# Performance work log

Measured on AMD Instinct MI355X. Metric: run time of the kernel, lower is better.

## Reference

```python
import jax, jax.numpy as jnp
import numpy as np

EPS = 1e-5
RS = 2                 # trilinear sampling points per bin per dim (fixed sampling_ratio)
OUT_SIZE = (4, 7, 7)   # (T_out, H_out, W_out)


def hswish(x):
    return x * jnp.clip(x + 3.0, 0.0, 6.0) / 6.0


def bn3d(x, g, b, m, v):
    # eval-mode BatchNorm3d over channel dim 1 of [N,C,T,H,W]
    s = g * jax.lax.rsqrt(v + EPS)
    return x * s[None, :, None, None, None] + (b - m * s)[None, :, None, None, None]


def conv3d(x, w, stride=1, pad=0, groups=1):
    return jax.lax.conv_general_dilated(
        x, w, window_strides=(stride,) * 3, padding=[(pad, pad)] * 3,
        dimension_numbers=('NCDHW', 'OIDHW', 'NCDHW'), feature_group_count=groups)


def roi_align_3d(feat, start, end):
    # feat: [N,C,T,H,W]; start/end: [N,3] in (x, y, t) order (one ROI per sample)
    N, C, T, H, W = feat.shape
    Pt, Ph, Pw = OUT_SIZE

    def coords(s, e, P):
        size = jnp.maximum(e - s, 1.0)
        # flattened sample j = bin*RS + i -> position s + (j+0.5)/RS * bin_size
        offs = (jnp.arange(P * RS, dtype=feat.dtype) + 0.5) / RS
        return s[:, None] + offs[None, :] * (size / P)[:, None]  # [N, P*RS]

    cx = coords(start[:, 0], end[:, 0], Pw)
    cy = coords(start[:, 1], end[:, 1], Ph)
    ct = coords(start[:, 2], end[:, 2], Pt)

    def lin(v, c, L):
        # linear interpolation of v along its last axis at continuous coords c
        c = jnp.clip(c, 0.0, L - 1.0)
        lo = jnp.floor(c).astype(jnp.int32)
        hi = jnp.minimum(lo + 1, L - 1)
        w = c - lo.astype(c.dtype)
        return v[..., lo] * (1.0 - w) + v[..., hi] * w

    def one(f, tt, ty, tx):
        f = lin(f, tx, W)                   # [C,T,H,Sw]
        f = jnp.moveaxis(f, 2, -1)          # [C,T,Sw,H]
        f = lin(f, ty, H)                   # [C,T,Sw,Sh]
        f = jnp.moveaxis(f, 1, -1)          # [C,Sw,Sh,T]
        f = lin(f, tt, T)                   # [C,Sw,Sh,St]
        f = jnp.transpose(f, (0, 3, 2, 1))  # [C,St,Sh,Sw]
        f = f.reshape(f.shape[0], Pt, RS, Ph, RS, Pw, RS)
        return f.mean(axis=(2, 4, 6))       # average sample points per bin

    return jax.vmap(one)(feat, ct, cy, cx)  # [N,C,Pt,Ph,Pw]


def setup_inputs():
    key = jax.random.key(0)
    ks = jax.random.split(key, 9)
    N, Cin, T, H, W = 64, 256, 8, 16, 16
    Cr = 128

    def bn_params(k, c):
        k1, k2, k3, k4 = jax.random.split(k, 4)
        g = jax.random.uniform(k1, (c,), minval=0.5, maxval=1.5)
        b = 0.1 * jax.random.normal(k2, (c,))
        m = 0.1 * jax.random.normal(k3, (c,))
        v = jax.random.uniform(k4, (c,), minval=0.5, maxval=1.5)
        return g, b, m, v

    x = jax.random.normal(ks[0], (N, Cin, T, H, W), jnp.float32)
    w1 = jax.random.normal(ks[1], (Cr, Cin, 1, 1, 1)) / np.float32(np.sqrt(Cin))
    wdw = jax.random.normal(ks[2], (Cr, 1, 3, 3, 3)) / np.float32(np.sqrt(27))
    w2 = jax.random.normal(ks[3], (Cr, Cr, 1, 1, 1)) / np.float32(np.sqrt(Cr))
    w3 = jax.random.normal(ks[4], (6, Cr, 1, 1, 1)) / np.float32(np.sqrt(Cr))
    g1, b1, m1, v1 = bn_params(ks[5], Cr)
    g2, b2, m2, v2 = bn_params(ks[6], Cr)
    g3, b3, m3, v3 = bn_params(ks[7], Cr)
    g4, b4, m4, v4 = bn_params(ks[8], 6)
    return dict(x=x, w1=w1, g1=g1, b1=b1, m1=m1, v1=v1,
                wdw=wdw, g2=g2, b2=b2, m2=m2, v2=v2,
                w2=w2, g3=g3, b3=b3, m3=m3, v3=v3,
                w3=w3, g4=g4, b4=b4, m4=m4, v4=v4)


def reference(x, w1, g1, b1, m1, v1, wdw, g2, b2, m2, v2,
              w2, g3, b3, m3, v3, w3, g4, b4, m4, v4):
    N, C, T, H, W = x.shape
    h = hswish(bn3d(conv3d(x, w1), g1, b1, m1, v1))
    h = hswish(bn3d(conv3d(h, wdw, stride=2, pad=1, groups=wdw.shape[0]), g2, b2, m2, v2))
    h = hswish(bn3d(conv3d(h, w2), g3, b3, m3, v3))
    # AvgPool3d with kernel == reduced feature size -> global spatial-temporal mean
    h = jnp.mean(h, axis=(2, 3, 4), keepdims=True)
    logits = bn3d(conv3d(h, w3), g4, b4, m4, v4).reshape(N, 6)
    lim = jax.nn.sigmoid(logits)   # eval path (gumbel only in training)
    scales = jnp.array([W, H, T], dtype=x.dtype)      # (x, y, t) order
    start = 0.5 * lim[:, :3] * scales
    end = (1.0 - 0.5 * lim[:, 3:]) * scales
    return roi_align_3d(x, start, end)
```

## Files before the change

### kernel.cpp

```cpp
#include <hip/hip_runtime.h>
#include <math.h>

#define N_BATCH 64
#define CIN 256
#define CR 128
#define T_IN 8
#define H_IN 16
#define W_IN 16
#define S1 2048
#define T2 4
#define H2 8
#define W2 8
#define S2 256
#define PT 4
#define PH 7
#define PW 7
#define EPSB 1e-5f

typedef __attribute__((ext_vector_type(8))) short bf16x8;
typedef __attribute__((ext_vector_type(4))) float f32x4;
typedef __attribute__((ext_vector_type(4))) unsigned int u32x4;
typedef __attribute__((ext_vector_type(8))) unsigned short ushort8;

__device__ __forceinline__ float hswish(float y) {
    float c = fminf(fmaxf(y + 3.0f, 0.0f), 6.0f);
    return y * c * (1.0f / 6.0f);
}

__device__ __forceinline__ unsigned int fbits(float x) {
    return __float_as_uint(x);
}

__device__ __forceinline__ unsigned int pkbf16(float lo, float hi) {
    return ((fbits(lo) + 0x8000u) >> 16) | ((fbits(hi) + 0x8000u) & 0xFFFF0000u);
}

__global__ __launch_bounds__(256) void wsplit_kernel(
    const float* __restrict__ w1, unsigned short* __restrict__ whi,
    unsigned short* __restrict__ wlo, float* __restrict__ pp)
{
    int i = blockIdx.x * 256 + threadIdx.x;
    int co = i >> 8;
    int k  = i & 255;
    float x = w1[i];
    unsigned int bx = fbits(x);
    unsigned int h = (bx + 0x8000u) & 0xFFFF0000u;
    float r = x - __uint_as_float(h);
    int flat = ((((co >> 4) * 8 + (k >> 5)) * 4 + ((k >> 3) & 3)) * 16 + (co & 15)) * 8 + (k & 7);
    whi[flat] = (unsigned short)(h >> 16);
    wlo[flat] = (unsigned short)((fbits(r) + 0x8000u) >> 16);
    pp[i] = 0.0f;
}

#define BFIDX(g, h, e, ln) (((((g) * 2 + (h)) * 2 + (e)) * 16 + (ln)) * 4)

__global__ __launch_bounds__(256, 5) void conv1_mfma_kernel(
    const float* __restrict__ x,
    const unsigned short* __restrict__ whi, const unsigned short* __restrict__ wlo,
    const float* __restrict__ g, const float* __restrict__ b,
    const float* __restrict__ m, const float* __restrict__ v,
    unsigned short* __restrict__ h1b)
{
    __shared__ unsigned int Bf[2][1024];

    int blk = blockIdx.x;
    int n  = blk >> 5;
    int s0 = (blk & 31) << 6;
    int tid = threadIdx.x;
    int wave = tid >> 6;
    int lane = tid & 63;
    int gl   = lane >> 4;
    int ln16 = lane & 15;
    int hw   = wave & 1;
    int wcoG = (wave >> 1) * 4;

    int sg = tid >> 6;
    int sc = tid & 63;
    int sh = sc >> 5;
    int se = sc & 1;
    int sl = (sc & 31) >> 1;
    int wslot = BFIDX(sg, sh, se, sl);
    const float* xg = x + (size_t)n * CIN * S1 + s0 + sc;

    f32x4 acc[4][2];
    #pragma unroll
    for (int i = 0; i < 4; i++) {
        acc[i][0] = (f32x4){0.f, 0.f, 0.f, 0.f};
        acc[i][1] = (f32x4){0.f, 0.f, 0.f, 0.f};
    }

    float val[3][8];
    #pragma unroll
    for (int j = 0; j < 8; j++)
        val[0][j] = xg[(size_t)(sg * 8 + j) * S1];
    #pragma unroll
    for (int j = 0; j < 8; j++)
        val[1][j] = xg[(size_t)(32 + sg * 8 + j) * S1];
    {
        u32x4 wv;
        #pragma unroll
        for (int p = 0; p < 4; p++)
            wv[p] = pkbf16(val[0][2 * p], val[0][2 * p + 1]);
        *reinterpret_cast<u32x4*>(&Bf[0][wslot]) = wv;
    }
    __syncthreads();

    #pragma unroll
    for (int ks = 0; ks < 8; ks++) {
        bf16x8 Ah[4], Al[4];
        #pragma unroll
        for (int fc = 0; fc < 4; fc++) {
            int off = ((((wcoG + fc) * 8 + ks) * 4 + gl) * 16 + ln16) * 8;
            Ah[fc] = *reinterpret_cast<const bf16x8*>(whi + off);
            Al[fc] = *reinterpret_cast<const bf16x8*>(wlo + off);
        }
        if (ks < 6) {
            #pragma unroll
            for (int j = 0; j < 8; j++)
                val[(ks + 2) % 3][j] = xg[(size_t)((ks + 2) * 32 + sg * 8 + j) * S1];
        }
        if (ks < 7) {
            u32x4 wv;
            #pragma unroll
            for (int p = 0; p < 4; p++)
                wv[p] = pkbf16(val[(ks + 1) % 3][2 * p], val[(ks + 1) % 3][2 * p + 1]);
            *reinterpret_cast<u32x4*>(&Bf[(ks + 1) & 1][wslot]) = wv;
        }
        union { u32x4 u; bf16x8 bv; } B0, B1;
        B0.u = *reinterpret_cast<const u32x4*>(&Bf[ks & 1][BFIDX(gl, hw, 0, ln16)]);
        B1.u = *reinterpret_cast<const u32x4*>(&Bf[ks & 1][BFIDX(gl, hw, 1, ln16)]);
        #pragma unroll
        for (int fc = 0; fc < 4; fc++) {
            acc[fc][0] = __builtin_amdgcn_mfma_f32_16x16x32_bf16(Ah[fc], B0.bv, acc[fc][0], 0, 0, 0);
            acc[fc][1] = __builtin_amdgcn_mfma_f32_16x16x32_bf16(Ah[fc], B1.bv, acc[fc][1], 0, 0, 0);
        }
        #pragma unroll
        for (int fc = 0; fc < 4; fc++) {
            acc[fc][0] = __builtin_amdgcn_mfma_f32_16x16x32_bf16(Al[fc], B0.bv, acc[fc][0], 0, 0, 0);
            acc[fc][1] = __builtin_amdgcn_mfma_f32_16x16x32_bf16(Al[fc], B1.bv, acc[fc][1], 0, 0, 0);
        }
        if (ks < 7) __syncthreads();
    }

    #pragma unroll
    for (int fc = 0; fc < 4; fc++)
        #pragma unroll
        for (int reg = 0; reg < 4; reg++) {
            int co = (wcoG + fc) * 16 + gl * 4 + reg;
            float sc_ = g[co] * rsqrtf(v[co] + EPSB);
            float tt = fmaf(-m[co], sc_, b[co]);
            float y0 = hswish(fmaf(acc[fc][0][reg], sc_, tt));
            float y1 = hswish(fmaf(acc[fc][1][reg], sc_, tt));
            unsigned int pk = pkbf16(y0, y1);
            *reinterpret_cast<unsigned int*>(
                h1b + ((size_t)n * CR + co) * S1 + s0 + hw * 32 + ln16 * 2) = pk;
        }
}

__global__ __launch_bounds__(256) void dwconv_kernel(
    const unsigned short* __restrict__ h1b, const float* __restrict__ wdw,
    const float* __restrict__ g, const float* __restrict__ b,
    const float* __restrict__ m, const float* __restrict__ v,
    float* __restrict__ h2)
{
    __shared__ float s[T_IN][H_IN][W_IN];
    __shared__ float wl[27];
    int blk = blockIdx.x;
    int n = blk >> 7;
    int c = blk & 127;
    int tid = threadIdx.x;
    const unsigned short* in = h1b + ((size_t)n * CR + c) * S1;

    {
        int e = tid * 8;
        ushort8 u = *reinterpret_cast<const ushort8*>(in + e);
        float* sp = &s[0][0][0] + e;
        #pragma unroll
        for (int i = 0; i < 8; i++)
            sp[i] = __uint_as_float((unsigned int)(unsigned short)u[i] << 16);
    }
    if (tid < 27) wl[tid] = wdw[c * 27 + tid];
    __syncthreads();

    int wo = tid & 7;
    int ho = (tid >> 3) & 7;
    int to = tid >> 6;
    float acc = 0.0f;
    #pragma unroll
    for (int dt = 0; dt < 3; dt++) {
        int ti = 2 * to - 1 + dt;
        if (ti < 0 || ti >= T_IN) continue;
        #pragma unroll
        for (int dh = 0; dh < 3; dh++) {
            int hi = 2 * ho - 1 + dh;
            if (hi < 0 || hi >= H_IN) continue;
            #pragma unroll
            for (int dw = 0; dw < 3; dw++) {
                int wi = 2 * wo - 1 + dw;
                if (wi < 0 || wi >= W_IN) continue;
                acc = fmaf(wl[(dt * 3 + dh) * 3 + dw], s[ti][hi][wi], acc);
            }
        }
    }
    float sc = g[c] * rsqrtf(v[c] + EPSB);
    float y  = fmaf(acc, sc, fmaf(-m[c], sc, b[c]));
    h2[((size_t)n * CR + c) * S2 + tid] = hswish(y);
}

#define KC 16
__global__ __launch_bounds__(256) void conv2_kernel(
    const float* __restrict__ h2, const float* __restrict__ w2,
    const float* __restrict__ g, const float* __restrict__ b,
    const float* __restrict__ m, const float* __restrict__ v,
    float* __restrict__ pp)
{
    __shared__ float Xs[KC][64];
    __shared__ float Ws[KC][CR + 4];

    int blk = blockIdx.x;
    int n  = blk >> 2;
    int sq = blk & 3;
    int s0 = sq << 6;
    int tid = threadIdx.x;
    int tco = tid >> 3;
    int ts  = tid & 7;
    const float* xn = h2 + (size_t)n * CR * S2;

    float acc[4][8];
    #pragma unroll
    for (int i = 0; i < 4; i++)
        #pragma unroll
        for (int j = 0; j < 8; j++) acc[i][j] = 0.0f;

    for (int k0 = 0; k0 < CR; k0 += KC) {
        {
            int e  = tid * 4;
            int kk = e >> 6;
            int ss = e & 63;
            float4 xv = *reinterpret_cast<const float4*>(xn + (size_t)(k0 + kk) * S2 + s0 + ss);
            *reinterpret_cast<float4*>(&Xs[kk][ss]) = xv;
        }
        #pragma unroll
        for (int r = 0; r < 8; r++) {
            int e  = tid + r * 256;
            int co = e >> 4;
            int kk = e & 15;
            Ws[kk][co] = w2[co * CR + k0 + kk];
        }
        __syncthreads();
        #pragma unroll
        for (int kk = 0; kk < KC; kk++) {
            float a[4], bb[8];
            #pragma unroll
            for (int r = 0; r < 4; r++) a[r] = Ws[kk][tco * 4 + r];
            #pragma unroll
            for (int q = 0; q < 8; q++) bb[q] = Xs[kk][ts * 8 + q];
            #pragma unroll
            for (int r = 0; r < 4; r++)
                #pragma unroll
                for (int q = 0; q < 8; q++)
                    acc[r][q] = fmaf(a[r], bb[q], acc[r][q]);
        }
        __syncthreads();
    }

    #pragma unroll
    for (int r = 0; r < 4; r++) {
        int co = tco * 4 + r;
        float sc = g[co] * rsqrtf(v[co] + EPSB);
        float tt = fmaf(-m[co], sc, b[co]);
        float psum = 0.0f;
        #pragma unroll
        for (int q = 0; q < 8; q++)
            psum += hswish(fmaf(acc[r][q], sc, tt));
        #pragma unroll
        for (int off = 4; off > 0; off >>= 1)
            psum += __shfl_down(psum, off, 8);
        if (ts == 0)
            pp[((size_t)n * CR + co) * 4 + sq] = psum;
    }
}

__global__ __launch_bounds__(128) void head_kernel(
    const float* __restrict__ pp, const float* __restrict__ w3,
    const float* __restrict__ g, const float* __restrict__ b,
    const float* __restrict__ m, const float* __restrict__ v,
    float* __restrict__ boxes)
{
    __shared__ float red[2];
    int n = blockIdx.x;
    int c = threadIdx.x;
    int wave = c >> 6, lane = c & 63;
    const float* p = pp + ((size_t)n * CR + c) * 4;
    float pc = (p[0] + p[1] + p[2] + p[3]) * (1.0f / 256.0f);

    for (int j = 0; j < 6; j++) {
        float t = w3[j * CR + c] * pc;
        #pragma unroll
        for (int off = 32; off > 0; off >>= 1)
            t += __shfl_down(t, off, 64);
        if (lane == 0) red[wave] = t;
        __syncthreads();
        if (c == 0) {
            float acc = red[0] + red[1];
            float sc = g[j] * rsqrtf(v[j] + EPSB);
            float logit = fmaf(acc, sc, fmaf(-m[j], sc, b[j]));
            float lim = 1.0f / (1.0f + expf(-logit));
            float scale = ((j % 3) == 2) ? 8.0f : 16.0f;
            float val = (j < 3) ? 0.5f * lim * scale : (1.0f - 0.5f * lim) * scale;
            boxes[n * 6 + j] = val;
        }
        __syncthreads();
    }
}

__global__ __launch_bounds__(256) void roi_kernel(
    const float* __restrict__ x, const float* __restrict__ boxes,
    float* __restrict__ out)
{
    __shared__ float s[T_IN][H_IN][W_IN];
    __shared__ float box[6];
    int blk = blockIdx.x;
    int n = blk >> 8;
    int c = blk & 255;
    int tid = threadIdx.x;
    const float* in = x + ((size_t)n * CIN + c) * S1;
    #pragma unroll
    for (int r = 0; r < 2; r++) {
        int e = (tid + r * 256) * 4;
        *reinterpret_cast<float4*>(&s[0][0][0] + e) =
            *reinterpret_cast<const float4*>(in + e);
    }
    if (tid < 6) box[tid] = boxes[n * 6 + tid];
    __syncthreads();

    if (tid < PT * PH * PW) {
        int pw = tid % 7;
        int ph = (tid / 7) % 7;
        int pt = tid / 49;
        float sx = box[0], sy = box[1], st = box[2];
        float bszx = fmaxf(box[3] - sx, 1.0f) * (1.0f / PW);
        float bszy = fmaxf(box[4] - sy, 1.0f) * (1.0f / PH);
        float bszt = fmaxf(box[5] - st, 1.0f) * (1.0f / PT);

        float acc = 0.0f;
        #pragma unroll
        for (int it = 0; it < 2; it++) {
            float tc = st + ((float)(pt * 2 + it) + 0.5f) * 0.5f * bszt;
            tc = fminf(fmaxf(tc, 0.0f), (float)(T_IN - 1));
            int tlo = (int)floorf(tc);
            int thi = min(tlo + 1, T_IN - 1);
            float tw = tc - (float)tlo;
            #pragma unroll
            for (int iy = 0; iy < 2; iy++) {
                float yc = sy + ((float)(ph * 2 + iy) + 0.5f) * 0.5f * bszy;
                yc = fminf(fmaxf(yc, 0.0f), (float)(H_IN - 1));
                int ylo = (int)floorf(yc);
                int yhi = min(ylo + 1, H_IN - 1);
                float yw = yc - (float)ylo;
                #pragma unroll
                for (int ix = 0; ix < 2; ix++) {
                    float xc = sx + ((float)(pw * 2 + ix) + 0.5f) * 0.5f * bszx;
                    xc = fminf(fmaxf(xc, 0.0f), (float)(W_IN - 1));
                    int xlo = (int)floorf(xc);
                    int xhi = min(xlo + 1, W_IN - 1);
                    float xw = xc - (float)xlo;

                    float v00 = s[tlo][ylo][xlo] * (1.0f - xw) + s[tlo][ylo][xhi] * xw;
                    float v01 = s[tlo][yhi][xlo] * (1.0f - xw) + s[tlo][yhi][xhi] * xw;
                    float v10 = s[thi][ylo][xlo] * (1.0f - xw) + s[thi][ylo][xhi] * xw;
                    float v11 = s[thi][yhi][xlo] * (1.0f - xw) + s[thi][yhi][xhi] * xw;
                    float v0 = v00 * (1.0f - yw) + v01 * yw;
                    float v1 = v10 * (1.0f - yw) + v11 * yw;
                    acc += v0 * (1.0f - tw) + v1 * tw;
                }
            }
        }
        out[(((size_t)(n * CIN + c) * PT + pt) * PH + ph) * PW + pw] = acc * 0.125f;
    }
}

extern "C" void kernel_launch(void* const* d_in, const int* in_sizes, int n_in,
                              void* d_out, int out_size, void* d_ws, size_t ws_size,
                              hipStream_t stream) {
    const float* x   = (const float*)d_in[0];
    const float* w1  = (const float*)d_in[1];
    const float* g1  = (const float*)d_in[2];
    const float* b1  = (const float*)d_in[3];
    const float* m1  = (const float*)d_in[4];
    const float* v1  = (const float*)d_in[5];
    const float* wdw = (const float*)d_in[6];
    const float* g2  = (const float*)d_in[7];
    const float* b2  = (const float*)d_in[8];
    const float* m2  = (const float*)d_in[9];
    const float* v2  = (const float*)d_in[10];
    const float* w2  = (const float*)d_in[11];
    const float* g3  = (const float*)d_in[12];
    const float* b3  = (const float*)d_in[13];
    const float* m3  = (const float*)d_in[14];
    const float* v3  = (const float*)d_in[15];
    const float* w3  = (const float*)d_in[16];
    const float* g4  = (const float*)d_in[17];
    const float* b4  = (const float*)d_in[18];
    const float* m4  = (const float*)d_in[19];
    const float* v4  = (const float*)d_in[20];

    float* ws = (float*)d_ws;
    float* h1     = ws;
    float* h2     = h1 + (size_t)N_BATCH * CR * S1;
    float* h3     = h2 + (size_t)N_BATCH * CR * S2;
    float* pp     = h3 + (size_t)N_BATCH * CR * S2;
    float* boxes  = pp + (size_t)N_BATCH * CR * 4;
    unsigned short* h1b = (unsigned short*)h1;
    unsigned short* whi = (unsigned short*)h3;
    unsigned short* wlo = whi + CR * CIN;

    wsplit_kernel<<<dim3(128), dim3(256), 0, stream>>>(w1, whi, wlo, pp);
    conv1_mfma_kernel<<<dim3(2048), dim3(256), 0, stream>>>(x, whi, wlo, g1, b1, m1, v1, h1b);
    dwconv_kernel<<<dim3(N_BATCH * CR), dim3(256), 0, stream>>>(h1b, wdw, g2, b2, m2, v2, h2);
    conv2_kernel<<<dim3(256), dim3(256), 0, stream>>>(h2, w2, g3, b3, m3, v3, pp);
    head_kernel<<<dim3(N_BATCH), dim3(128), 0, stream>>>(pp, w3, g4, b4, m4, v4, boxes);
    roi_kernel<<<dim3(N_BATCH * CIN), dim3(256), 0, stream>>>(x, boxes, (float*)d_out);
}
```

Measured before the change: 125.3 us.

## Pre-convert input to channel-packed bf16 layout and drop LDS staging in conv1

Adds a separate kernel that converts x from fp32 into bf16 packed in groups of 8 channels per spatial position. conv1 then loads its MFMA B operands straight from global memory, with no shared-memory double buffering and no barriers. The aim is to remove the strided fp32 loads, the in-loop packing and the synchronisation from conv1. In exchange it adds a kernel launch plus an extra full write and read of x in bf16 (about 67MB of fp32 read and 33MB written), lowers the occupancy hint from 5 to 4, and repacks the workspace layout.

New measurement: 152.7 us. 21.9% more time.

```diff
diff --git a/kernel.cpp b/kernel.cpp
--- a/kernel.cpp
+++ b/kernel.cpp
@@ -52,17 +52,37 @@
     pp[i] = 0.0f;
 }
 
-#define BFIDX(g, h, e, ln) (((((g) * 2 + (h)) * 2 + (e)) * 16 + (ln)) * 4)
-
-__global__ __launch_bounds__(256, 5) void conv1_mfma_kernel(
-    const float* __restrict__ x,
+__global__ __launch_bounds__(256) void xcvt_kernel(
+    const float* __restrict__ x, unsigned short* __restrict__ xb8)
+{
+    int blk = blockIdx.x;
+    int n   = blk >> 5;
+    int ci8 = blk & 31;
+    int t = threadIdx.x;
+    const float* xr = x + ((size_t)n * CIN + ci8 * 8) * S1;
+    unsigned short* ob = xb8 + (size_t)blk * S1 * 8;
+    #pragma unroll
+    for (int i = 0; i < 8; i++) {
+        int s = i * 256 + t;
+        float vj[8];
+        #pragma unroll
+        for (int j = 0; j < 8; j++)
+            vj[j] = xr[(size_t)j * S1 + s];
+        u32x4 pk;
+        #pragma unroll
+        for (int p = 0; p < 4; p++)
+            pk[p] = pkbf16(vj[2 * p], vj[2 * p + 1]);
+        *reinterpret_cast<u32x4*>(ob + (size_t)s * 8) = pk;
+    }
+}
+
+__global__ __launch_bounds__(256, 4) void conv1_mfma_kernel(
+    const unsigned short* __restrict__ xb8,
     const unsigned short* __restrict__ whi, const unsigned short* __restrict__ wlo,
     const float* __restrict__ g, const float* __restrict__ b,
     const float* __restrict__ m, const float* __restrict__ v,
     unsigned short* __restrict__ h1b)
 {
-    __shared__ unsigned int Bf[2][1024];
-
     int blk = blockIdx.x;
     int n  = blk >> 5;
     int s0 = (blk & 31) << 6;
@@ -74,13 +94,8 @@
     int hw   = wave & 1;
     int wcoG = (wave >> 1) * 4;
 
-    int sg = tid >> 6;
-    int sc = tid & 63;
-    int sh = sc >> 5;
-    int se = sc & 1;
-    int sl = (sc & 31) >> 1;
-    int wslot = BFIDX(sg, sh, se, sl);
-    const float* xg = x + (size_t)n * CIN * S1 + s0 + sc;
+    const unsigned short* xb = xb8 +
+        (((size_t)n * 32 + gl) * S1 + s0 + hw * 32 + 2 * ln16) * 8;
 
     f32x4 acc[4][2];
     #pragma unroll
@@ -89,24 +104,10 @@
         acc[i][1] = (f32x4){0.f, 0.f, 0.f, 0.f};
     }
 
-    float val[3][8];
-    #pragma unroll
-    for (int j = 0; j < 8; j++)
-        val[0][j] = xg[(size_t)(sg * 8 + j) * S1];
-    #pragma unroll
-    for (int j = 0; j < 8; j++)
-        val[1][j] = xg[(size_t)(32 + sg * 8 + j) * S1];
-    {
-        u32x4 wv;
-        #pragma unroll
-        for (int p = 0; p < 4; p++)
-            wv[p] = pkbf16(val[0][2 * p], val[0][2 * p + 1]);
-        *reinterpret_cast<u32x4*>(&Bf[0][wslot]) = wv;
-    }
-    __syncthreads();
-
     #pragma unroll
     for (int ks = 0; ks < 8; ks++) {
+        bf16x8 B0 = *reinterpret_cast<const bf16x8*>(xb + (size_t)(ks * 4) * S1 * 8);
+        bf16x8 B1 = *reinterpret_cast<const bf16x8*>(xb + (size_t)(ks * 4) * S1 * 8 + 8);
         bf16x8 Ah[4], Al[4];
         #pragma unroll
         for (int fc = 0; fc < 4; fc++) {
@@ -114,32 +115,16 @@
             Ah[fc] = *reinterpret_cast<const bf16x8*>(whi + off);
             Al[fc] = *reinterpret_cast<const bf16x8*>(wlo + off);
         }
-        if (ks < 6) {
-            #pragma unroll
-            for (int j = 0; j < 8; j++)
-                val[(ks + 2) % 3][j] = xg[(size_t)((ks + 2) * 32 + sg * 8 + j) * S1];
-        }
-        if (ks < 7) {
-            u32x4 wv;
-            #pragma unroll
-            for (int p = 0; p < 4; p++)
-                wv[p] = pkbf16(val[(ks + 1) % 3][2 * p], val[(ks + 1) % 3][2 * p + 1]);
-            *reinterpret_cast<u32x4*>(&Bf[(ks + 1) & 1][wslot]) = wv;
-        }
-        union { u32x4 u; bf16x8 bv; } B0, B1;
-        B0.u = *reinterpret_cast<const u32x4*>(&Bf[ks & 1][BFIDX(gl, hw, 0, ln16)]);
-        B1.u = *reinterpret_cast<const u32x4*>(&Bf[ks & 1][BFIDX(gl, hw, 1, ln16)]);
         #pragma unroll
         for (int fc = 0; fc < 4; fc++) {
-            acc[fc][0] = __builtin_amdgcn_mfma_f32_16x16x32_bf16(Ah[fc], B0.bv, acc[fc][0], 0, 0, 0);
-            acc[fc][1] = __builtin_amdgcn_mfma_f32_16x16x32_bf16(Ah[fc], B1.bv, acc[fc][1], 0, 0, 0);
+            acc[fc][0] = __builtin_amdgcn_mfma_f32_16x16x32_bf16(Ah[fc], B0, acc[fc][0], 0, 0, 0);
+            acc[fc][1] = __builtin_amdgcn_mfma_f32_16x16x32_bf16(Ah[fc], B1, acc[fc][1], 0, 0, 0);
         }
         #pragma unroll
         for (int fc = 0; fc < 4; fc++) {
-            acc[fc][0] = __builtin_amdgcn_mfma_f32_16x16x32_bf16(Al[fc], B0.bv, acc[fc][0], 0, 0, 0);
-            acc[fc][1] = __builtin_amdgcn_mfma_f32_16x16x32_bf16(Al[fc], B1.bv, acc[fc][1], 0, 0, 0);
-        }
-        if (ks < 7) __syncthreads();
+            acc[fc][0] = __builtin_amdgcn_mfma_f32_16x16x32_bf16(Al[fc], B0, acc[fc][0], 0, 0, 0);
+            acc[fc][1] = __builtin_amdgcn_mfma_f32_16x16x32_bf16(Al[fc], B1, acc[fc][1], 0, 0, 0);
+        }
     }
 
     #pragma unroll
@@ -405,18 +390,17 @@
     const float* m4  = (const float*)d_in[19];
     const float* v4  = (const float*)d_in[20];
 
-    float* ws = (float*)d_ws;
-    float* h1     = ws;
-    float* h2     = h1 + (size_t)N_BATCH * CR * S1;
-    float* h3     = h2 + (size_t)N_BATCH * CR * S2;
-    float* pp     = h3 + (size_t)N_BATCH * CR * S2;
-    float* boxes  = pp + (size_t)N_BATCH * CR * 4;
-    unsigned short* h1b = (unsigned short*)h1;
-    unsigned short* whi = (unsigned short*)h3;
+    unsigned short* xb8 = (unsigned short*)d_ws;
+    unsigned short* h1b = xb8 + (size_t)N_BATCH * 32 * S1 * 8;
+    float* h2   = (float*)(h1b + (size_t)N_BATCH * CR * S1);
+    unsigned short* whi = (unsigned short*)(h2 + (size_t)N_BATCH * CR * S2);
     unsigned short* wlo = whi + CR * CIN;
+    float* pp    = (float*)(wlo + CR * CIN);
+    float* boxes = pp + (size_t)N_BATCH * CR * 4;
 
     wsplit_kernel<<<dim3(128), dim3(256), 0, stream>>>(w1, whi, wlo, pp);
-    conv1_mfma_kernel<<<dim3(2048), dim3(256), 0, stream>>>(x, whi, wlo, g1, b1, m1, v1, h1b);
+    xcvt_kernel<<<dim3(2048), dim3(256), 0, stream>>>(x, xb8);
+    conv1_mfma_kernel<<<dim3(2048), dim3(256), 0, stream>>>(xb8, whi, wlo, g1, b1, m1, v1, h1b);
     dwconv_kernel<<<dim3(N_BATCH * CR), dim3(256), 0, stream>>>(h1b, wdw, g2, b2, m2, v2, h2);
     conv2_kernel<<<dim3(256), dim3(256), 0, stream>>>(h2, w2, g3, b3, m3, v3, pp);
     head_kernel<<<dim3(N_BATCH), dim3(128), 0, stream>>>(pp, w3, g4, b4, m4, v4, boxes);
```

## Remap conv1 waves to own 32 output channels and preload all weight fragments

Applied to the files above, without the earlier changes.

Each wave now covers 32 output channels across all 64 spatial columns, instead of 64 channels across 32 columns. Its whole slice of the hi/lo bf16 weight fragments is loaded into registers before the K loop. This takes global weight loads out of the inner loop and reuses each weight fragment across four B tiles. The cost is much higher register pressure, so the launch bound drops from 5 to 2 blocks per SM, which lowers occupancy and the ability to hide the x-load latency.

New measurement: 118.9 us. 5.1% less time.

```diff
diff --git a/kernel.cpp b/kernel.cpp
--- a/kernel.cpp
+++ b/kernel.cpp
@@ -54,7 +54,7 @@
 
 #define BFIDX(g, h, e, ln) (((((g) * 2 + (h)) * 2 + (e)) * 16 + (ln)) * 4)
 
-__global__ __launch_bounds__(256, 5) void conv1_mfma_kernel(
+__global__ __launch_bounds__(256, 2) void conv1_mfma_kernel(
     const float* __restrict__ x,
     const unsigned short* __restrict__ whi, const unsigned short* __restrict__ wlo,
     const float* __restrict__ g, const float* __restrict__ b,
@@ -71,23 +71,29 @@
     int lane = tid & 63;
     int gl   = lane >> 4;
     int ln16 = lane & 15;
-    int hw   = wave & 1;
-    int wcoG = (wave >> 1) * 4;
 
     int sg = tid >> 6;
     int sc = tid & 63;
-    int sh = sc >> 5;
-    int se = sc & 1;
-    int sl = (sc & 31) >> 1;
-    int wslot = BFIDX(sg, sh, se, sl);
+    int wslot = BFIDX(sg, sc >> 5, sc & 1, (sc & 31) >> 1);
     const float* xg = x + (size_t)n * CIN * S1 + s0 + sc;
 
-    f32x4 acc[4][2];
-    #pragma unroll
-    for (int i = 0; i < 4; i++) {
-        acc[i][0] = (f32x4){0.f, 0.f, 0.f, 0.f};
-        acc[i][1] = (f32x4){0.f, 0.f, 0.f, 0.f};
-    }
+    bf16x8 Ah[2][8], Al[2][8];
+    #pragma unroll
+    for (int fc = 0; fc < 2; fc++)
+        #pragma unroll
+        for (int ks = 0; ks < 8; ks++) {
+            int coG = wave * 2 + fc;
+            int off = (((coG * 8 + ks) * 4 + gl) * 16 + ln16) * 8;
+            Ah[fc][ks] = *reinterpret_cast<const bf16x8*>(whi + off);
+            Al[fc][ks] = *reinterpret_cast<const bf16x8*>(wlo + off);
+        }
+
+    f32x4 acc[2][4];
+    #pragma unroll
+    for (int i = 0; i < 2; i++)
+        #pragma unroll
+        for (int j = 0; j < 4; j++)
+            acc[i][j] = (f32x4){0.f, 0.f, 0.f, 0.f};
 
     float val[3][8];
     #pragma unroll
@@ -107,13 +113,6 @@
 
     #pragma unroll
     for (int ks = 0; ks < 8; ks++) {
-        bf16x8 Ah[4], Al[4];
-        #pragma unroll
-        for (int fc = 0; fc < 4; fc++) {
-            int off = ((((wcoG + fc) * 8 + ks) * 4 + gl) * 16 + ln16) * 8;
-            Ah[fc] = *reinterpret_cast<const bf16x8*>(whi + off);
-            Al[fc] = *reinterpret_cast<const bf16x8*>(wlo + off);
-        }
         if (ks < 6) {
             #pragma unroll
             for (int j = 0; j < 8; j++)
@@ -126,34 +125,40 @@
                 wv[p] = pkbf16(val[(ks + 1) % 3][2 * p], val[(ks + 1) % 3][2 * p + 1]);
             *reinterpret_cast<u32x4*>(&Bf[(ks + 1) & 1][wslot]) = wv;
         }
-        union { u32x4 u; bf16x8 bv; } B0, B1;
-        B0.u = *reinterpret_cast<const u32x4*>(&Bf[ks & 1][BFIDX(gl, hw, 0, ln16)]);
-        B1.u = *reinterpret_cast<const u32x4*>(&Bf[ks & 1][BFIDX(gl, hw, 1, ln16)]);
-        #pragma unroll
-        for (int fc = 0; fc < 4; fc++) {
-            acc[fc][0] = __builtin_amdgcn_mfma_f32_16x16x32_bf16(Ah[fc], B0.bv, acc[fc][0], 0, 0, 0);
-            acc[fc][1] = __builtin_amdgcn_mfma_f32_16x16x32_bf16(Ah[fc], B1.bv, acc[fc][1], 0, 0, 0);
-        }
-        #pragma unroll
-        for (int fc = 0; fc < 4; fc++) {
-            acc[fc][0] = __builtin_amdgcn_mfma_f32_16x16x32_bf16(Al[fc], B0.bv, acc[fc][0], 0, 0, 0);
-            acc[fc][1] = __builtin_amdgcn_mfma_f32_16x16x32_bf16(Al[fc], B1.bv, acc[fc][1], 0, 0, 0);
-        }
+        union { u32x4 u; bf16x8 bv; } B[4];
+        #pragma unroll
+        for (int fs = 0; fs < 4; fs++)
+            B[fs].u = *reinterpret_cast<const u32x4*>(
+                &Bf[ks & 1][BFIDX(gl, fs >> 1, fs & 1, ln16)]);
+        #pragma unroll
+        for (int fc = 0; fc < 2; fc++)
+            #pragma unroll
+            for (int fs = 0; fs < 4; fs++)
+                acc[fc][fs] = __builtin_amdgcn_mfma_f32_16x16x32_bf16(
+                    Ah[fc][ks], B[fs].bv, acc[fc][fs], 0, 0, 0);
+        #pragma unroll
+        for (int fc = 0; fc < 2; fc++)
+            #pragma unroll
+            for (int fs = 0; fs < 4; fs++)
+                acc[fc][fs] = __builtin_amdgcn_mfma_f32_16x16x32_bf16(
+                    Al[fc][ks], B[fs].bv, acc[fc][fs], 0, 0, 0);
         if (ks < 7) __syncthreads();
     }
 
     #pragma unroll
-    for (int fc = 0; fc < 4; fc++)
+    for (int fc = 0; fc < 2; fc++)
         #pragma unroll
         for (int reg = 0; reg < 4; reg++) {
-            int co = (wcoG + fc) * 16 + gl * 4 + reg;
+            int co = wave * 32 + fc * 16 + gl * 4 + reg;
             float sc_ = g[co] * rsqrtf(v[co] + EPSB);
             float tt = fmaf(-m[co], sc_, b[co]);
             float y0 = hswish(fmaf(acc[fc][0][reg], sc_, tt));
             float y1 = hswish(fmaf(acc[fc][1][reg], sc_, tt));
-            unsigned int pk = pkbf16(y0, y1);
-            *reinterpret_cast<unsigned int*>(
-                h1b + ((size_t)n * CR + co) * S1 + s0 + hw * 32 + ln16 * 2) = pk;
+            float y2 = hswish(fmaf(acc[fc][2][reg], sc_, tt));
+            float y3 = hswish(fmaf(acc[fc][3][reg], sc_, tt));
+            unsigned short* o = h1b + ((size_t)n * CR + co) * S1 + s0;
+            *reinterpret_cast<unsigned int*>(o + 2 * ln16)      = pkbf16(y0, y1);
+            *reinterpret_cast<unsigned int*>(o + 32 + 2 * ln16) = pkbf16(y2, y3);
         }
 }
 
```

## Load conv1 input directly into registers, dropping LDS staging and barriers

Applied to the files above, without the earlier changes.

The conv1 MFMA kernel no longer stages the activation tile through shared memory with double buffering and per-step barriers. Each lane now loads all 64 of its input float2 values up front and packs them to bf16 MFMA B operands in registers. Launch bounds drop to 2 blocks per CU to make room for the much larger register footprint. Waves sharing the same input columns now load duplicate data from global memory (or L2), and lower occupancy can hurt latency hiding.

Measured after the change: 127.0 us. Within noise of the previous version (+1.3%).

```diff
diff --git a/kernel.cpp b/kernel.cpp
--- a/kernel.cpp
+++ b/kernel.cpp
@@ -52,17 +52,13 @@
     pp[i] = 0.0f;
 }
 
-#define BFIDX(g, h, e, ln) (((((g) * 2 + (h)) * 2 + (e)) * 16 + (ln)) * 4)
-
-__global__ __launch_bounds__(256, 5) void conv1_mfma_kernel(
+__global__ __launch_bounds__(256, 2) void conv1_mfma_kernel(
     const float* __restrict__ x,
     const unsigned short* __restrict__ whi, const unsigned short* __restrict__ wlo,
     const float* __restrict__ g, const float* __restrict__ b,
     const float* __restrict__ m, const float* __restrict__ v,
     unsigned short* __restrict__ h1b)
 {
-    __shared__ unsigned int Bf[2][1024];
-
     int blk = blockIdx.x;
     int n  = blk >> 5;
     int s0 = (blk & 31) << 6;
@@ -74,13 +70,25 @@
     int hw   = wave & 1;
     int wcoG = (wave >> 1) * 4;
 
-    int sg = tid >> 6;
-    int sc = tid & 63;
-    int sh = sc >> 5;
-    int se = sc & 1;
-    int sl = (sc & 31) >> 1;
-    int wslot = BFIDX(sg, sh, se, sl);
-    const float* xg = x + (size_t)n * CIN * S1 + s0 + sc;
+    const float* xg = x + (size_t)n * CIN * S1 + s0 + hw * 32 + 2 * ln16;
+
+    union BU { u32x4 u; bf16x8 bv; } B[8][2];
+    {
+        float2 st[8][8];
+        #pragma unroll
+        for (int ks = 0; ks < 8; ks++)
+            #pragma unroll
+            for (int j = 0; j < 8; j++)
+                st[ks][j] = *reinterpret_cast<const float2*>(
+                    xg + (size_t)(ks * 32 + gl * 8 + j) * S1);
+        #pragma unroll
+        for (int ks = 0; ks < 8; ks++)
+            #pragma unroll
+            for (int p = 0; p < 4; p++) {
+                B[ks][0].u[p] = pkbf16(st[ks][2 * p].x, st[ks][2 * p + 1].x);
+                B[ks][1].u[p] = pkbf16(st[ks][2 * p].y, st[ks][2 * p + 1].y);
+            }
+    }
 
     f32x4 acc[4][2];
     #pragma unroll
@@ -88,22 +96,6 @@
         acc[i][0] = (f32x4){0.f, 0.f, 0.f, 0.f};
         acc[i][1] = (f32x4){0.f, 0.f, 0.f, 0.f};
     }
-
-    float val[3][8];
-    #pragma unroll
-    for (int j = 0; j < 8; j++)
-        val[0][j] = xg[(size_t)(sg * 8 + j) * S1];
-    #pragma unroll
-    for (int j = 0; j < 8; j++)
-        val[1][j] = xg[(size_t)(32 + sg * 8 + j) * S1];
-    {
-        u32x4 wv;
-        #pragma unroll
-        for (int p = 0; p < 4; p++)
-            wv[p] = pkbf16(val[0][2 * p], val[0][2 * p + 1]);
-        *reinterpret_cast<u32x4*>(&Bf[0][wslot]) = wv;
-    }
-    __syncthreads();
 
     #pragma unroll
     for (int ks = 0; ks < 8; ks++) {
@@ -114,32 +106,16 @@
             Ah[fc] = *reinterpret_cast<const bf16x8*>(whi + off);
             Al[fc] = *reinterpret_cast<const bf16x8*>(wlo + off);
         }
-        if (ks < 6) {
-            #pragma unroll
-            for (int j = 0; j < 8; j++)
-                val[(ks + 2) % 3][j] = xg[(size_t)((ks + 2) * 32 + sg * 8 + j) * S1];
-        }
-        if (ks < 7) {
-            u32x4 wv;
-            #pragma unroll
-            for (int p = 0; p < 4; p++)
-                wv[p] = pkbf16(val[(ks + 1) % 3][2 * p], val[(ks + 1) % 3][2 * p + 1]);
-            *reinterpret_cast<u32x4*>(&Bf[(ks + 1) & 1][wslot]) = wv;
-        }
-        union { u32x4 u; bf16x8 bv; } B0, B1;
-        B0.u = *reinterpret_cast<const u32x4*>(&Bf[ks & 1][BFIDX(gl, hw, 0, ln16)]);
-        B1.u = *reinterpret_cast<const u32x4*>(&Bf[ks & 1][BFIDX(gl, hw, 1, ln16)]);
         #pragma unroll
         for (int fc = 0; fc < 4; fc++) {
-            acc[fc][0] = __builtin_amdgcn_mfma_f32_16x16x32_bf16(Ah[fc], B0.bv, acc[fc][0], 0, 0, 0);
-            acc[fc][1] = __builtin_amdgcn_mfma_f32_16x16x32_bf16(Ah[fc], B1.bv, acc[fc][1], 0, 0, 0);
+            acc[fc][0] = __builtin_amdgcn_mfma_f32_16x16x32_bf16(Ah[fc], B[ks][0].bv, acc[fc][0], 0, 0, 0);
+            acc[fc][1] = __builtin_amdgcn_mfma_f32_16x16x32_bf16(Ah[fc], B[ks][1].bv, acc[fc][1], 0, 0, 0);
         }
         #pragma unroll
         for (int fc = 0; fc < 4; fc++) {
-            acc[fc][0] = __builtin_amdgcn_mfma_f32_16x16x32_bf16(Al[fc], B0.bv, acc[fc][0], 0, 0, 0);
-            acc[fc][1] = __builtin_amdgcn_mfma_f32_16x16x32_bf16(Al[fc], B1.bv, acc[fc][1], 0, 0, 0);
-        }
-        if (ks < 7) __syncthreads();
+            acc[fc][0] = __builtin_amdgcn_mfma_f32_16x16x32_bf16(Al[fc], B[ks][0].bv, acc[fc][0], 0, 0, 0);
+            acc[fc][1] = __builtin_amdgcn_mfma_f32_16x16x32_bf16(Al[fc], B[ks][1].bv, acc[fc][1], 0, 0, 0);
+        }
     }
 
     #pragma unroll
```
